# Kernel tuning notes

Hardware: AMD Instinct MI355X
Metric: run time of the kernel (lower is better)

Reference implementation:

```python
import jax
import jax.numpy as jnp
import numpy as np
from jax import lax

B, T, D = 32, 256, 512   # batch, seq len, controller_dim (== memory_dim)
S = 2048                 # memory_slots
EPS_LN = 1e-5            # nn.LayerNorm default eps
EPS_NRM = 1e-12          # F.normalize default eps


def setup_inputs() -> dict:
    key = jax.random.key(0)
    ks = jax.random.split(key, 12)
    sc = 1.0 / np.sqrt(D)  # roughly torch Linear init scale
    return {
        "controller_seq": jax.random.normal(ks[0], (B, T, D), dtype=jnp.float32),
        "memory": jax.random.normal(ks[1], (S, D), dtype=jnp.float32),
        "Wk": jax.random.normal(ks[2], (D, D), dtype=jnp.float32) * sc,
        "bk": jax.random.normal(ks[3], (D,), dtype=jnp.float32) * sc,
        "We": jax.random.normal(ks[4], (D, D), dtype=jnp.float32) * sc,
        "be": jax.random.normal(ks[5], (D,), dtype=jnp.float32) * sc,
        "Ww": jax.random.normal(ks[6], (D, D), dtype=jnp.float32) * sc,
        "bw": jax.random.normal(ks[7], (D,), dtype=jnp.float32) * sc,
        "Wg": jax.random.normal(ks[8], (D, D), dtype=jnp.float32) * sc,
        "bg": jax.random.normal(ks[9], (D,), dtype=jnp.float32) * sc,
        "gamma": jnp.ones((D,), dtype=jnp.float32),
        "beta": jnp.zeros((D,), dtype=jnp.float32),
    }


def _l2norm(x, axis=-1):
    # matches F.normalize: x / max(||x||, eps)
    n = jnp.sqrt(jnp.sum(x * x, axis=axis, keepdims=True))
    return x / jnp.maximum(n, EPS_NRM)


def _layernorm(x, gamma, beta):
    mu = jnp.mean(x, axis=-1, keepdims=True)
    var = jnp.mean((x - mu) ** 2, axis=-1, keepdims=True)
    return (x - mu) * lax.rsqrt(var + EPS_LN) * gamma + beta


def reference(controller_seq, memory, Wk, bk, We, be, Ww, bw, Wg, bg, gamma, beta):
    batch = controller_seq.shape[0]

    def step(mem, c):  # mem: [S, Dm], c: [B, Dc]
        # --- read (addressing by cosine similarity) ---
        k = c @ Wk.T + bk                       # [B, Dm]
        sim = _l2norm(k) @ _l2norm(mem).T       # [B, S]
        w = jax.nn.softmax(sim, axis=-1)        # [B, S]
        read_val = w @ mem                      # [B, Dm]
        # --- write (erase / add, averaged over batch) ---
        erase = jax.nn.sigmoid(c @ We.T + be)   # [B, Dm]
        add = c @ Ww.T + bw                     # [B, Dm]
        # mean_b (1 - w_bs * e_bd) = 1 - (w^T e)/B ; avoids [B,S,Dm] intermediate
        erase_m = 1.0 - jnp.einsum("bs,bd->sd", w, erase) / batch
        add_m = jnp.einsum("bs,bd->sd", w, add) / batch
        new_mem = _layernorm(mem * erase_m + add_m, gamma, beta)  # dropout in eval mode
        # --- gated output ---
        g = jax.nn.sigmoid(c @ Wg.T + bg)       # [B, Dm]
        out_t = g * c + (1.0 - g) * read_val
        return new_mem, out_t

    _, outs = lax.scan(step, memory, jnp.swapaxes(controller_seq, 0, 1))  # outs: [T, B, D]
    return jnp.swapaxes(outs, 0, 1)  # [B, T, D]
```

## Files before the change

kernel.cpp:

```cpp
#include <hip/hip_runtime.h>

#define DEV __device__ __forceinline__

namespace {
constexpr int Bc = 32;
constexpr int Tc = 256;
constexpr int Dc = 512;
constexpr int NBLK = 256;
constexpr int NW   = 128;
constexpr int ROWS = 16;

constexpr size_t OFF_KN   = 0;
constexpr size_t OFF_E    = OFF_KN + (size_t)Tc * Bc * Dc;
constexpr size_t OFF_A    = OFF_E  + (size_t)Tc * Bc * Dc;
constexpr size_t OFF_RP   = OFF_A  + (size_t)Tc * Bc * Dc;
constexpr size_t OFF_DENP = OFF_RP + (size_t)2 * NW * Bc * Dc;
constexpr size_t OFF_FLAGS= OFF_DENP + (size_t)2 * NW * Bc;
}

DEV float sigm(float x) { return 1.0f / (1.0f + __expf(-x)); }

DEV float ld1cg(const float* p) {
  unsigned u = __hip_atomic_load((const unsigned*)p, __ATOMIC_RELAXED,
                                 __HIP_MEMORY_SCOPE_AGENT);
  return __uint_as_float(u);
}
DEV void st1cg(float* p, float v) {
  __hip_atomic_store((unsigned*)p, __float_as_uint(v), __ATOMIC_RELAXED,
                     __HIP_MEMORY_SCOPE_AGENT);
}
DEV float2 ld2cg(const float* p) {
  unsigned long long u = __hip_atomic_load((const unsigned long long*)p,
                                           __ATOMIC_RELAXED, __HIP_MEMORY_SCOPE_AGENT);
  union { unsigned long long u; float2 f; } c; c.u = u; return c.f;
}
DEV void st2cg(float* p, float2 v) {
  union { float2 f; unsigned long long u; } c; c.f = v;
  __hip_atomic_store((unsigned long long*)p, c.u, __ATOMIC_RELAXED,
                     __HIP_MEMORY_SCOPE_AGENT);
}

__global__ __launch_bounds__(256) void k_gemm(
    const float* __restrict__ A,
    const float* __restrict__ Wk, const float* __restrict__ bk,
    const float* __restrict__ We, const float* __restrict__ be,
    const float* __restrict__ Ww, const float* __restrict__ bw,
    const float* __restrict__ Wg, const float* __restrict__ bg,
    float* __restrict__ ws, float* __restrict__ gout)
{
  __shared__ float As[32][68];
  __shared__ float Bs[32][68];

  const int bid = blockIdx.x;
  const int mat = bid >> 10;
  const int rem = bid & 1023;
  const int rt = rem >> 3, jt = rem & 7;
  const int rbase = rt * 64, jbase = jt * 64;

  const float* Wm; const float* bm;
  if      (mat == 0) { Wm = Wk; bm = bk; }
  else if (mat == 1) { Wm = We; bm = be; }
  else if (mat == 2) { Wm = Ww; bm = bw; }
  else               { Wm = Wg; bm = bg; }

  const int tid = threadIdx.x;
  const int lr = tid >> 2;
  const int lk = (tid & 3) * 8;
  const int ty = tid >> 4, tx = tid & 15;

  float acc[4][4] = {};

  for (int k0 = 0; k0 < Dc; k0 += 32) {
    const float4 a0 = *(const float4*)&A [(size_t)(rbase + lr) * Dc + k0 + lk];
    const float4 a1 = *(const float4*)&A [(size_t)(rbase + lr) * Dc + k0 + lk + 4];
    const float4 b0 = *(const float4*)&Wm[(size_t)(jbase + lr) * Dc + k0 + lk];
    const float4 b1 = *(const float4*)&Wm[(size_t)(jbase + lr) * Dc + k0 + lk + 4];
    __syncthreads();
    As[lk + 0][lr] = a0.x; As[lk + 1][lr] = a0.y; As[lk + 2][lr] = a0.z; As[lk + 3][lr] = a0.w;
    As[lk + 4][lr] = a1.x; As[lk + 5][lr] = a1.y; As[lk + 6][lr] = a1.z; As[lk + 7][lr] = a1.w;
    Bs[lk + 0][lr] = b0.x; Bs[lk + 1][lr] = b0.y; Bs[lk + 2][lr] = b0.z; Bs[lk + 3][lr] = b0.w;
    Bs[lk + 4][lr] = b1.x; Bs[lk + 5][lr] = b1.y; Bs[lk + 6][lr] = b1.z; Bs[lk + 7][lr] = b1.w;
    __syncthreads();
    #pragma unroll
    for (int kk = 0; kk < 32; ++kk) {
      const float4 av = *(const float4*)&As[kk][ty * 4];
      const float4 bv = *(const float4*)&Bs[kk][tx * 4];
      const float ar[4] = {av.x, av.y, av.z, av.w};
      const float br[4] = {bv.x, bv.y, bv.z, bv.w};
      #pragma unroll
      for (int i = 0; i < 4; ++i)
        #pragma unroll
        for (int j = 0; j < 4; ++j)
          acc[i][j] = fmaf(ar[i], br[j], acc[i][j]);
    }
  }

  const float4 bias = *(const float4*)&bm[jbase + tx * 4];
  const float bi[4] = {bias.x, bias.y, bias.z, bias.w};
  #pragma unroll
  for (int i = 0; i < 4; ++i) {
    const int r = rbase + ty * 4 + i;
    float v[4];
    #pragma unroll
    for (int j = 0; j < 4; ++j) {
      v[j] = acc[i][j] + bi[j];
      if (mat & 1) v[j] = sigm(v[j]);
    }
    float4 o; o.x = v[0]; o.y = v[1]; o.z = v[2]; o.w = v[3];
    if (mat == 3) {
      *(float4*)&gout[(size_t)r * Dc + jbase + tx * 4] = o;
    } else {
      float* dst = ws + (mat == 0 ? OFF_KN : (mat == 1 ? OFF_E : OFF_A));
      const int t = r & 255, b = r >> 8;
      *(float4*)&dst[((size_t)t * Bc + b) * Dc + jbase + tx * 4] = o;
    }
  }
}

__global__ __launch_bounds__(256) void k_knorm(float* __restrict__ kn)
{
  const int row = blockIdx.x * 4 + (threadIdx.x >> 6);
  const int lane = threadIdx.x & 63;
  float* p = kn + (size_t)row * Dc;
  float4 v0 = *(const float4*)&p[lane * 4];
  float4 v1 = *(const float4*)&p[256 + lane * 4];
  float ss = v0.x*v0.x + v0.y*v0.y + v0.z*v0.z + v0.w*v0.w
           + v1.x*v1.x + v1.y*v1.y + v1.z*v1.z + v1.w*v1.w;
  #pragma unroll
  for (int off = 32; off >= 1; off >>= 1) ss += __shfl_xor(ss, off);
  const float inv = 1.0f / fmaxf(sqrtf(ss), 1e-12f);
  v0.x *= inv; v0.y *= inv; v0.z *= inv; v0.w *= inv;
  v1.x *= inv; v1.y *= inv; v1.z *= inv; v1.w *= inv;
  *(float4*)&p[lane * 4] = v0;
  *(float4*)&p[256 + lane * 4] = v1;
}

DEV void gbar(unsigned* flags, unsigned step, int bid, int tid)
{
  __syncthreads();
  if (tid == 0)
    __hip_atomic_store(&flags[bid * 16], step, __ATOMIC_RELAXED,
                       __HIP_MEMORY_SCOPE_AGENT);
  while (__hip_atomic_load(&flags[tid * 16], __ATOMIC_RELAXED,
                           __HIP_MEMORY_SCOPE_AGENT) < step)
    __builtin_amdgcn_s_sleep(1);
  __syncthreads();
}

DEV void sim_phase(const float (*knb)[516], float* __restrict__ denp_row,
                   const float (*y)[516], float* __restrict__ ew_own,
                   const float* invn_s, float* sred, int tid)
{
  const int r = tid >> 4, bp = tid & 15;
  float acc0 = 0.f, acc1 = 0.f;
  #pragma unroll 4
  for (int dq = 0; dq < Dc / 4; ++dq) {
    const float4 y4 = *(const float4*)&y[r][dq * 4];
    const float4 ka = *(const float4*)&knb[bp][dq * 4];
    const float4 kb = *(const float4*)&knb[bp + 16][dq * 4];
    acc0 = fmaf(y4.x, ka.x, acc0); acc0 = fmaf(y4.y, ka.y, acc0);
    acc0 = fmaf(y4.z, ka.z, acc0); acc0 = fmaf(y4.w, ka.w, acc0);
    acc1 = fmaf(y4.x, kb.x, acc1); acc1 = fmaf(y4.y, kb.y, acc1);
    acc1 = fmaf(y4.z, kb.z, acc1); acc1 = fmaf(y4.w, kb.w, acc1);
  }
  const float iv = invn_s[r];
  const float e0 = __expf(acc0 * iv);
  const float e1 = __expf(acc1 * iv);
  ew_own[r * 32 + bp]      = e0;
  ew_own[r * 32 + bp + 16] = e1;
  if (tid < 32) sred[tid] = 0.f;
  __syncthreads();
  atomicAdd(&sred[bp], e0);
  atomicAdd(&sred[bp + 16], e1);
  __syncthreads();
  if (tid < 32) st1cg(&denp_row[tid], sred[tid]);
}

__global__ __launch_bounds__(256, 1) void k_main(
    const float* __restrict__ cs, const float* __restrict__ mem_in,
    const float* __restrict__ gamma, const float* __restrict__ beta,
    float* __restrict__ ws, float* __restrict__ out)
{
  __shared__ float mrows[16][516];
  __shared__ float knbuf[32][516];
  __shared__ float ew_own[16 * 32];
  __shared__ float wbuf[16][32];
  __shared__ float lds_red[256];
  __shared__ float2 red2[256];
  __shared__ float sred[32];
  __shared__ float mu_s[16], rs_s[16], invn_s[16], dinv_s[32];

  float* kn   = ws + OFF_KN;
  float* eptb = ws + OFF_E;
  float* aptb = ws + OFF_A;
  float* rp   = ws + OFF_RP;
  float* denp = ws + OFF_DENP;
  unsigned* flags = (unsigned*)(ws + OFF_FLAGS);

  const int bid = blockIdx.x, tid = threadIdx.x;
  const float inv32 = 1.0f / 32.0f;

  float2 ev[32], av[32];

  if (bid < NW) {
    const int s0 = bid * ROWS;
    const int c0 = tid * 2;
    #pragma unroll
    for (int r = 0; r < ROWS; ++r)
      *(float2*)&mrows[r][c0] = *(const float2*)&mem_in[(size_t)(s0 + r) * Dc + c0];
    #pragma unroll
    for (int i = 0; i < 16; ++i) {
      const int idx = tid + i * 256;
      const int row = idx >> 7, col = (idx & 127) * 4;
      *(float4*)&knbuf[row][col] = *(const float4*)&kn[row * Dc + col];
    }
    #pragma unroll
    for (int b = 0; b < 32; ++b) {
      ev[b] = *(const float2*)&eptb[(size_t)b * Dc + c0];
      av[b] = *(const float2*)&aptb[(size_t)b * Dc + c0];
    }
    __syncthreads();
    {
      const int row = tid >> 4, li = tid & 15;
      float ss = 0.f;
      #pragma unroll
      for (int i = 0; i < 8; ++i) {
        const float4 v = *(const float4*)&mrows[row][(li + i * 16) * 4];
        ss += v.x*v.x + v.y*v.y + v.z*v.z + v.w*v.w;
      }
      ss += __shfl_xor(ss, 8); ss += __shfl_xor(ss, 4);
      ss += __shfl_xor(ss, 2); ss += __shfl_xor(ss, 1);
      if (li == 0) invn_s[row] = 1.0f / fmaxf(sqrtf(ss), 1e-12f);
    }
    __syncthreads();
    sim_phase(knbuf, denp + (size_t)bid * Bc, mrows, ew_own, invn_s, sred, tid);
  }
  gbar(flags, 1u, bid, tid);

  for (int t = 0; t <= Tc; ++t) {
    if (bid < NW) {
      if (t < Tc) {
        const int c0 = tid * 2;
        if (t < Tc - 1) {
          const float* src = kn + (size_t)(t + 1) * Bc * Dc;
          #pragma unroll
          for (int i = 0; i < 16; ++i) {
            const int idx = tid + i * 256;
            const int row = idx >> 7, col = (idx & 127) * 4;
            *(float4*)&knbuf[row][col] = *(const float4*)&src[row * Dc + col];
          }
        }
        {
          const float* dp = denp + (size_t)(t & 1) * NW * Bc;
          const int b = tid & 31, ch = tid >> 5;
          float s = 0.f;
          #pragma unroll
          for (int g = 0; g < 16; ++g)
            s += ld1cg(&dp[(size_t)(ch * 16 + g) * Bc + b]);
          lds_red[tid] = s;
          __syncthreads();
          if (tid < 32) {
            float tot = 0.f;
            #pragma unroll
            for (int c2 = 0; c2 < 8; ++c2) tot += lds_red[c2 * 32 + tid];
            dinv_s[tid] = 1.0f / tot;
          }
          __syncthreads();
        }
        for (int idx = tid; idx < ROWS * 32; idx += 256)
          wbuf[idx >> 5][idx & 31] = ew_own[idx] * dinv_s[idx & 31];
        __syncthreads();

        float2 mr[ROWS];
        #pragma unroll
        for (int r = 0; r < ROWS; ++r) mr[r] = *(const float2*)&mrows[r][c0];
        {
          float* rpd = rp + (size_t)(t & 1) * NW * Bc * Dc
                          + (size_t)bid * Bc * Dc + c0;
          #pragma unroll 4
          for (int b = 0; b < 32; ++b) {
            float2 a; a.x = 0.f; a.y = 0.f;
            #pragma unroll
            for (int r = 0; r < ROWS; ++r) {
              const float wv = wbuf[r][b];
              a.x = fmaf(wv, mr[r].x, a.x);
              a.y = fmaf(wv, mr[r].y, a.y);
            }
            st2cg(rpd + (size_t)b * Dc, a);
          }
        }

        if (t < Tc - 1) {
          float2 er[ROWS] = {}, ad[ROWS] = {};
          #pragma unroll
          for (int b = 0; b < 32; ++b) {
            const float2 e2 = ev[b], a2 = av[b];
            #pragma unroll
            for (int r = 0; r < ROWS; ++r) {
              const float wv = wbuf[r][b];
              er[r].x = fmaf(wv, e2.x, er[r].x); er[r].y = fmaf(wv, e2.y, er[r].y);
              ad[r].x = fmaf(wv, a2.x, ad[r].x); ad[r].y = fmaf(wv, a2.y, ad[r].y);
            }
          }
          float2 xr[ROWS];
          #pragma unroll
          for (int r = 0; r < ROWS; ++r) {
            float2 x;
            x.x = mr[r].x * (1.0f - er[r].x * inv32) + ad[r].x * inv32;
            x.y = mr[r].y * (1.0f - er[r].y * inv32) + ad[r].y * inv32;
            xr[r] = x;
            *(float2*)&mrows[r][c0] = x;
          }
          if (t <= Tc - 3) {
            const float* ep1 = eptb + (size_t)(t + 1) * Bc * Dc;
            const float* ap1 = aptb + (size_t)(t + 1) * Bc * Dc;
            #pragma unroll
            for (int b = 0; b < 32; ++b) {
              ev[b] = *(const float2*)&ep1[(size_t)b * Dc + c0];
              av[b] = *(const float2*)&ap1[(size_t)b * Dc + c0];
            }
          }
          __syncthreads();
          {
            const int row = tid >> 4, li = tid & 15;
            float s1 = 0.f, s2 = 0.f;
            #pragma unroll
            for (int i = 0; i < 8; ++i) {
              const float4 v = *(const float4*)&mrows[row][(li + i * 16) * 4];
              s1 += v.x + v.y + v.z + v.w;
              s2 += v.x*v.x + v.y*v.y + v.z*v.z + v.w*v.w;
            }
            s1 += __shfl_xor(s1, 8); s2 += __shfl_xor(s2, 8);
            s1 += __shfl_xor(s1, 4); s2 += __shfl_xor(s2, 4);
            s1 += __shfl_xor(s1, 2); s2 += __shfl_xor(s2, 2);
            s1 += __shfl_xor(s1, 1); s2 += __shfl_xor(s2, 1);
            if (li == 0) {
              const float mu = s1 * (1.0f / 512.0f);
              const float var = s2 * (1.0f / 512.0f) - mu * mu;
              mu_s[row] = mu;
              rs_s[row] = rsqrtf(var + 1e-5f);
            }
          }
          __syncthreads();
          const float2 gm  = *(const float2*)&gamma[c0];
          const float2 bt2 = *(const float2*)&beta[c0];
          #pragma unroll
          for (int r = 0; r < ROWS; ++r) {
            const float mu = mu_s[r], rs = rs_s[r];
            float2 y;
            y.x = (xr[r].x - mu) * rs * gm.x + bt2.x;
            y.y = (xr[r].y - mu) * rs * gm.y + bt2.y;
            *(float2*)&mrows[r][c0] = y;
          }
          __syncthreads();
          {
            const int row = tid >> 4, li = tid & 15;
            float ss = 0.f;
            #pragma unroll
            for (int i = 0; i < 8; ++i) {
              const float4 v = *(const float4*)&mrows[row][(li + i * 16) * 4];
              ss += v.x*v.x + v.y*v.y + v.z*v.z + v.w*v.w;
            }
            ss += __shfl_xor(ss, 8); ss += __shfl_xor(ss, 4);
            ss += __shfl_xor(ss, 2); ss += __shfl_xor(ss, 1);
            if (li == 0) invn_s[row] = 1.0f / fmaxf(sqrtf(ss), 1e-12f);
          }
          __syncthreads();
          sim_phase(knbuf,
                    denp + (size_t)((t + 1) & 1) * NW * Bc + (size_t)bid * Bc,
                    mrows, ew_own, invn_s, sred, tid);
        }
      }
    } else {
      if (t >= 1) {
        const int t0 = t - 1;
        const int rb = bid - NW;
        const int b = rb >> 2;
        const int d0 = (rb & 3) * 128;
        const float* rpc = rp + (size_t)(t0 & 1) * NW * Bc * Dc
                              + (size_t)b * Dc + d0;
        const int jp = (tid & 63) * 2;
        const int q  = tid >> 6;
        float2 a; a.x = 0.f; a.y = 0.f;
        #pragma unroll 4
        for (int pi = 0; pi < 32; ++pi) {
          const int p = q * 32 + pi;
          const float2 v = ld2cg(rpc + (size_t)p * Bc * Dc + jp);
          a.x += v.x; a.y += v.y;
        }
        red2[tid] = a;
        __syncthreads();
        if (tid < 64) {
          const float2 v0 = red2[tid];
          const float2 v1 = red2[64 + tid];
          const float2 v2 = red2[128 + tid];
          const float2 v3 = red2[192 + tid];
          float2 rv;
          rv.x = (v0.x + v1.x) + (v2.x + v3.x);
          rv.y = (v0.y + v1.y) + (v2.y + v3.y);
          const size_t oofs = ((size_t)b * Tc + t0) * Dc + d0 + tid * 2;
          const float2 g  = *(const float2*)&out[oofs];
          const float2 cv = *(const float2*)&cs[oofs];
          float2 o;
          o.x = g.x * cv.x + (1.0f - g.x) * rv.x;
          o.y = g.y * cv.y + (1.0f - g.y) * rv.y;
          *(float2*)&out[oofs] = o;
        }
        __syncthreads();
      }
    }
    if (t < Tc) gbar(flags, (unsigned)(t + 2), bid, tid);
  }
}

extern "C" void kernel_launch(void* const* d_in, const int* in_sizes, int n_in,
                              void* d_out, int out_size, void* d_ws, size_t ws_size,
                              hipStream_t stream)
{
  const float* cs    = (const float*)d_in[0];
  const float* mem   = (const float*)d_in[1];
  const float* Wk    = (const float*)d_in[2];
  const float* bk    = (const float*)d_in[3];
  const float* We    = (const float*)d_in[4];
  const float* be    = (const float*)d_in[5];
  const float* Ww    = (const float*)d_in[6];
  const float* bw    = (const float*)d_in[7];
  const float* Wg    = (const float*)d_in[8];
  const float* bg    = (const float*)d_in[9];
  const float* gamma = (const float*)d_in[10];
  const float* beta  = (const float*)d_in[11];
  float* ws  = (float*)d_ws;
  float* out = (float*)d_out;

  hipMemsetAsync(ws + OFF_FLAGS, 0, 256 * 16 * sizeof(unsigned), stream);

  hipLaunchKernelGGL(k_gemm, dim3(4096), dim3(256), 0, stream,
                     cs, Wk, bk, We, be, Ww, bw, Wg, bg, ws, out);
  hipLaunchKernelGGL(k_knorm, dim3(2048), dim3(256), 0, stream, ws + OFF_KN);
  hipLaunchKernelGGL(k_main, dim3(NBLK), dim3(256), 0, stream,
                     cs, mem, gamma, beta, ws, out);
}
```

Before: 9.902 ms.

## Store read partials as bf16 and read keys directly from global memory

Per-block partial read vectors are now packed to bf16 in LDS and written to global as 8-byte words, halving the cross-block traffic that the reducer blocks sum every step. The reducer layout is reorganized so each thread accumulates eight columns over eight partials, followed by an LDS reduction. The per-step copy of the next key matrix into LDS is dropped, and the similarity phase reads keys straight from global memory. This trades accuracy of the read value for less memory traffic, and relies on L2 or cache hits for the key loads.

```diff
diff --git a/kernel.cpp b/kernel.cpp
--- a/kernel.cpp
+++ b/kernel.cpp
@@ -29,16 +29,21 @@
   __hip_atomic_store((unsigned*)p, __float_as_uint(v), __ATOMIC_RELAXED,
                      __HIP_MEMORY_SCOPE_AGENT);
 }
-DEV float2 ld2cg(const float* p) {
-  unsigned long long u = __hip_atomic_load((const unsigned long long*)p,
-                                           __ATOMIC_RELAXED, __HIP_MEMORY_SCOPE_AGENT);
-  union { unsigned long long u; float2 f; } c; c.u = u; return c.f;
-}
-DEV void st2cg(float* p, float2 v) {
-  union { float2 f; unsigned long long u; } c; c.f = v;
-  __hip_atomic_store((unsigned long long*)p, c.u, __ATOMIC_RELAXED,
-                     __HIP_MEMORY_SCOPE_AGENT);
-}
+DEV unsigned long long ld8cg(const unsigned long long* p) {
+  return __hip_atomic_load(p, __ATOMIC_RELAXED, __HIP_MEMORY_SCOPE_AGENT);
+}
+DEV void st8cg(unsigned long long* p, unsigned long long v) {
+  __hip_atomic_store(p, v, __ATOMIC_RELAXED, __HIP_MEMORY_SCOPE_AGENT);
+}
+
+DEV unsigned pack_bf2(float x, float y) {
+  unsigned ux = __float_as_uint(x), uy = __float_as_uint(y);
+  unsigned rx = (ux + 0x7FFFu + ((ux >> 16) & 1u)) >> 16;
+  unsigned ry = (uy + 0x7FFFu + ((uy >> 16) & 1u)) >> 16;
+  return rx | (ry << 16);
+}
+DEV float lo16f(unsigned u) { return __uint_as_float(u << 16); }
+DEV float hi16f(unsigned u) { return __uint_as_float(u & 0xFFFF0000u); }
 
 __global__ __launch_bounds__(256) void k_gemm(
     const float* __restrict__ A,
@@ -147,17 +152,19 @@
   __syncthreads();
 }
 
-DEV void sim_phase(const float (*knb)[516], float* __restrict__ denp_row,
+DEV void sim_phase(const float* __restrict__ knp, float* __restrict__ denp_row,
                    const float (*y)[516], float* __restrict__ ew_own,
                    const float* invn_s, float* sred, int tid)
 {
   const int r = tid >> 4, bp = tid & 15;
+  const float* k0p = knp + (size_t)bp * Dc;
+  const float* k1p = knp + (size_t)(bp + 16) * Dc;
   float acc0 = 0.f, acc1 = 0.f;
   #pragma unroll 4
   for (int dq = 0; dq < Dc / 4; ++dq) {
     const float4 y4 = *(const float4*)&y[r][dq * 4];
-    const float4 ka = *(const float4*)&knb[bp][dq * 4];
-    const float4 kb = *(const float4*)&knb[bp + 16][dq * 4];
+    const float4 ka = *(const float4*)&k0p[dq * 4];
+    const float4 kb = *(const float4*)&k1p[dq * 4];
     acc0 = fmaf(y4.x, ka.x, acc0); acc0 = fmaf(y4.y, ka.y, acc0);
     acc0 = fmaf(y4.z, ka.z, acc0); acc0 = fmaf(y4.w, ka.w, acc0);
     acc1 = fmaf(y4.x, kb.x, acc1); acc1 = fmaf(y4.y, kb.y, acc1);
@@ -181,24 +188,25 @@
     const float* __restrict__ gamma, const float* __restrict__ beta,
     float* __restrict__ ws, float* __restrict__ out)
 {
-  __shared__ float mrows[16][516];
-  __shared__ float knbuf[32][516];
-  __shared__ float ew_own[16 * 32];
-  __shared__ float wbuf[16][32];
-  __shared__ float lds_red[256];
-  __shared__ float2 red2[256];
-  __shared__ float sred[32];
-  __shared__ float mu_s[16], rs_s[16], invn_s[16], dinv_s[32];
+  __shared__ float    mrows[16][516];
+  __shared__ unsigned sbuf[32][256];
+  __shared__ float    ew_own[16 * 32];
+  __shared__ float    wbuf[16][32];
+  __shared__ float    lds_red[256];
+  __shared__ float    redR[16][128];
+  __shared__ float    sred[32];
+  __shared__ float    mu_s[16], rs_s[16], invn_s[16], dinv_s[32];
 
   float* kn   = ws + OFF_KN;
   float* eptb = ws + OFF_E;
   float* aptb = ws + OFF_A;
-  float* rp   = ws + OFF_RP;
+  unsigned long long* rp64_all = (unsigned long long*)(ws + OFF_RP);
   float* denp = ws + OFF_DENP;
   unsigned* flags = (unsigned*)(ws + OFF_FLAGS);
 
   const int bid = blockIdx.x, tid = threadIdx.x;
   const float inv32 = 1.0f / 32.0f;
+  const size_t RPPAR = (size_t)NW * Bc * (Dc / 4);
 
   float2 ev[32], av[32];
 
@@ -208,12 +216,6 @@
     #pragma unroll
     for (int r = 0; r < ROWS; ++r)
       *(float2*)&mrows[r][c0] = *(const float2*)&mem_in[(size_t)(s0 + r) * Dc + c0];
-    #pragma unroll
-    for (int i = 0; i < 16; ++i) {
-      const int idx = tid + i * 256;
-      const int row = idx >> 7, col = (idx & 127) * 4;
-      *(float4*)&knbuf[row][col] = *(const float4*)&kn[row * Dc + col];
-    }
     #pragma unroll
     for (int b = 0; b < 32; ++b) {
       ev[b] = *(const float2*)&eptb[(size_t)b * Dc + c0];
@@ -233,7 +235,7 @@
       if (li == 0) invn_s[row] = 1.0f / fmaxf(sqrtf(ss), 1e-12f);
     }
     __syncthreads();
-    sim_phase(knbuf, denp + (size_t)bid * Bc, mrows, ew_own, invn_s, sred, tid);
+    sim_phase(kn, denp + (size_t)bid * Bc, mrows, ew_own, invn_s, sred, tid);
   }
   gbar(flags, 1u, bid, tid);
 
@@ -241,15 +243,6 @@
     if (bid < NW) {
       if (t < Tc) {
         const int c0 = tid * 2;
-        if (t < Tc - 1) {
-          const float* src = kn + (size_t)(t + 1) * Bc * Dc;
-          #pragma unroll
-          for (int i = 0; i < 16; ++i) {
-            const int idx = tid + i * 256;
-            const int row = idx >> 7, col = (idx & 127) * 4;
-            *(float4*)&knbuf[row][col] = *(const float4*)&src[row * Dc + col];
-          }
-        }
         {
           const float* dp = denp + (size_t)(t & 1) * NW * Bc;
           const int b = tid & 31, ch = tid >> 5;
@@ -274,19 +267,29 @@
         float2 mr[ROWS];
         #pragma unroll
         for (int r = 0; r < ROWS; ++r) mr[r] = *(const float2*)&mrows[r][c0];
+        #pragma unroll 4
+        for (int b = 0; b < 32; ++b) {
+          float2 a; a.x = 0.f; a.y = 0.f;
+          #pragma unroll
+          for (int r = 0; r < ROWS; ++r) {
+            const float wv = wbuf[r][b];
+            a.x = fmaf(wv, mr[r].x, a.x);
+            a.y = fmaf(wv, mr[r].y, a.y);
+          }
+          sbuf[b][tid] = pack_bf2(a.x, a.y);
+        }
+        __syncthreads();
         {
-          float* rpd = rp + (size_t)(t & 1) * NW * Bc * Dc
-                          + (size_t)bid * Bc * Dc + c0;
-          #pragma unroll 4
-          for (int b = 0; b < 32; ++b) {
-            float2 a; a.x = 0.f; a.y = 0.f;
-            #pragma unroll
-            for (int r = 0; r < ROWS; ++r) {
-              const float wv = wbuf[r][b];
-              a.x = fmaf(wv, mr[r].x, a.x);
-              a.y = fmaf(wv, mr[r].y, a.y);
-            }
-            st2cg(rpd + (size_t)b * Dc, a);
+          unsigned long long* rp64 = rp64_all + (size_t)(t & 1) * RPPAR
+                                   + (size_t)bid * Bc * (Dc / 4);
+          #pragma unroll
+          for (int i = 0; i < 16; ++i) {
+            const int idx = tid + i * 256;
+            const int b = idx >> 7, dq = idx & 127;
+            const unsigned long long v =
+                (unsigned long long)sbuf[b][dq * 2]
+              | ((unsigned long long)sbuf[b][dq * 2 + 1] << 32);
+            st8cg(&rp64[(size_t)b * (Dc / 4) + dq], v);
           }
         }
 
@@ -366,7 +369,7 @@
             if (li == 0) invn_s[row] = 1.0f / fmaxf(sqrtf(ss), 1e-12f);
           }
           __syncthreads();
-          sim_phase(knbuf,
+          sim_phase(kn + (size_t)(t + 1) * Bc * Dc,
                     denp + (size_t)((t + 1) & 1) * NW * Bc + (size_t)bid * Bc,
                     mrows, ew_own, invn_s, sred, tid);
         }
@@ -377,34 +380,35 @@
         const int rb = bid - NW;
         const int b = rb >> 2;
         const int d0 = (rb & 3) * 128;
-        const float* rpc = rp + (size_t)(t0 & 1) * NW * Bc * Dc
-                              + (size_t)b * Dc + d0;
-        const int jp = (tid & 63) * 2;
-        const int q  = tid >> 6;
-        float2 a; a.x = 0.f; a.y = 0.f;
-        #pragma unroll 4
-        for (int pi = 0; pi < 32; ++pi) {
-          const int p = q * 32 + pi;
-          const float2 v = ld2cg(rpc + (size_t)p * Bc * Dc + jp);
-          a.x += v.x; a.y += v.y;
-        }
-        red2[tid] = a;
+        const unsigned long long* rp64 = rp64_all + (size_t)(t0 & 1) * RPPAR;
+        const int pg = tid >> 4;
+        const int cq = tid & 15;
+        const size_t cofs = (size_t)(d0 + cq * 8) / 4;
+        float acc[8] = {};
+        #pragma unroll
+        for (int i = 0; i < 8; ++i) {
+          const int p = pg * 8 + i;
+          const size_t base = ((size_t)p * Bc + b) * (Dc / 4) + cofs;
+          const unsigned long long v0 = ld8cg(&rp64[base]);
+          const unsigned long long v1 = ld8cg(&rp64[base + 1]);
+          const unsigned u0 = (unsigned)v0, u1 = (unsigned)(v0 >> 32);
+          const unsigned u2 = (unsigned)v1, u3 = (unsigned)(v1 >> 32);
+          acc[0] += lo16f(u0); acc[1] += hi16f(u0);
+          acc[2] += lo16f(u1); acc[3] += hi16f(u1);
+          acc[4] += lo16f(u2); acc[5] += hi16f(u2);
+          acc[6] += lo16f(u3); acc[7] += hi16f(u3);
+        }
+        #pragma unroll
+        for (int j = 0; j < 8; ++j) redR[pg][cq * 8 + j] = acc[j];
         __syncthreads();
-        if (tid < 64) {
-          const float2 v0 = red2[tid];
-          const float2 v1 = red2[64 + tid];
-          const float2 v2 = red2[128 + tid];
-          const float2 v3 = red2[192 + tid];
-          float2 rv;
-          rv.x = (v0.x + v1.x) + (v2.x + v3.x);
-          rv.y = (v0.y + v1.y) + (v2.y + v3.y);
-          const size_t oofs = ((size_t)b * Tc + t0) * Dc + d0 + tid * 2;
-          const float2 g  = *(const float2*)&out[oofs];
-          const float2 cv = *(const float2*)&cs[oofs];
-          float2 o;
-          o.x = g.x * cv.x + (1.0f - g.x) * rv.x;
-          o.y = g.y * cv.y + (1.0f - g.y) * rv.y;
-          *(float2*)&out[oofs] = o;
+        if (tid < 128) {
+          float s = 0.f;
+          #pragma unroll
+          for (int p = 0; p < 16; ++p) s += redR[p][tid];
+          const size_t oofs = ((size_t)b * Tc + t0) * Dc + d0 + tid;
+          const float g  = out[oofs];
+          const float cv = cs[oofs];
+          out[oofs] = g * cv + (1.0f - g) * s;
         }
         __syncthreads();
       }
```

Measured after the change: 12.23 ms. +23.6%, slower.
